# Performance work log

Hardware: AMD Instinct MI355X
Metric: run time of the kernel (lower is better)

## Reference

```python
import jax, jax.numpy as jnp
import numpy as np
from jax import lax

N, C_IN, H, W = 32, 128, 64, 64
C_OUT, KH, KW = 256, 3, 3
C_DIM = 64


def setup_inputs() -> dict:
    key = jax.random.key(0)
    k1, k2, k3, k4, k5 = jax.random.split(key, 5)
    return {
        "x": jax.random.normal(k1, (N, C_IN, H, W), dtype=jnp.float32),
        "c": jax.random.normal(k2, (N, C_DIM), dtype=jnp.float32),
        "weight": jax.random.normal(k3, (C_OUT, C_IN, KH, KW), dtype=jnp.float32),
        "c_weight": jax.random.normal(k4, (C_OUT, C_DIM), dtype=jnp.float32),
        "bias": jax.random.normal(k5, (C_OUT,), dtype=jnp.float32),
    }


def reference(x, c, weight, c_weight, bias):
    # Equivalent to the module's unfold + matmul path (groups=1, dilation=1,
    # zero padding=1, stride=1): a direct conv fused with the spatially
    # invariant context bias c @ c_weight^T and the channel bias.
    out = lax.conv_general_dilated(
        x, weight,
        window_strides=(1, 1),
        padding=((1, 1), (1, 1)),
        dimension_numbers=("NCHW", "OIHW", "NCHW"),
    )  # (N, C_out, H, W)
    ctx = jnp.einsum("nd,od->no", c, c_weight)  # (N, C_out), same at every spatial loc
    return out + ctx[:, :, None, None] + bias[None, :, None, None]
```

## Files before the change

### kernel.cpp

```cpp
#include <hip/hip_runtime.h>
#include <hip/hip_bf16.h>


#define NN   32
#define CIN  128
#define HH   64
#define WW   64
#define COUT 256
#define CDIM 64
#define HP   66
#define WP   66

#define XP_BYTES  ((size_t)NN*HP*WP*CIN*2)
#define WT_BYTES  ((size_t)9*COUT*CIN*2)
#define CTX_BYTES ((size_t)NN*COUT*4)
#define WS_NEEDED (XP_BYTES + WT_BYTES + CTX_BYTES)

typedef __attribute__((ext_vector_type(8))) short short8;
typedef __attribute__((ext_vector_type(4))) float float4v;

__device__ __forceinline__ void async16(const void* g, void* l) {
    __builtin_amdgcn_global_load_lds(
        (const __attribute__((address_space(1))) unsigned int*)g,
        (__attribute__((address_space(3))) unsigned int*)l, 16, 0, 0);
}

__global__ __launch_bounds__(256) void prep_x(const float* __restrict__ x,
                                              __hip_bfloat16* __restrict__ xP) {
    __shared__ float tile[CIN][WW + 1];
    int n = blockIdx.x >> 6;
    int h = blockIdx.x & 63;
    int t = threadIdx.x;
    const float* xp = x + ((size_t)n * CIN) * (HH * WW) + h * WW;
    int w = t & 63, cib = t >> 6;
    #pragma unroll
    for (int i = 0; i < 32; ++i) {
        int ci = cib + i * 4;
        tile[ci][w] = xp[(size_t)ci * (HH * WW) + w];
    }
    __syncthreads();
    int w2 = t >> 2, cseg = (t & 3) * 32;
    __hip_bfloat16* dst = xP + (((size_t)n * HP + (h + 1)) * WP + (w2 + 1)) * CIN + cseg;
    #pragma unroll
    for (int j = 0; j < 32; ++j)
        dst[j] = __float2bfloat16(tile[cseg + j][w2]);
}

__global__ __launch_bounds__(256) void prep_w(const float* __restrict__ wgt,
                                              __hip_bfloat16* __restrict__ wT) {
    int idx = blockIdx.x * 256 + threadIdx.x;
    int ci  = idx & 127;
    int co  = (idx >> 7) & 255;
    int tap = idx >> 15;
    wT[idx] = __float2bfloat16(wgt[((size_t)co * CIN + ci) * 9 + tap]);
}

__global__ __launch_bounds__(256) void prep_ctx(const float* __restrict__ c,
                                                const float* __restrict__ cw,
                                                const float* __restrict__ bias,
                                                float* __restrict__ ctx) {
    int idx = blockIdx.x * 256 + threadIdx.x;
    int co = idx & 255, n = idx >> 8;
    float a = bias[co];
    #pragma unroll 8
    for (int d = 0; d < CDIM; ++d) a += c[n * CDIM + d] * cw[co * CDIM + d];
    ctx[idx] = a;
}

__global__ __launch_bounds__(256) void conv_mfma(
    const __hip_bfloat16* __restrict__ xP,
    const __hip_bfloat16* __restrict__ wT,
    const float* __restrict__ ctx,
    float* __restrict__ out)
{
    __shared__ __align__(16) short A_s[4096];
    __shared__ __align__(16) short B_s[4096];

    int bid = blockIdx.x;
    int nt  = bid & 1;
    int mt  = bid >> 1;
    int n   = mt >> 5;
    int h0  = (mt & 31) << 1;

    int tid = threadIdx.x;
    int lane = tid & 63, wv = tid >> 6;
    int m0 = (wv & 1) * 64, n0 = (wv >> 1) * 64;

    int prow = wv * 32 + (lane >> 2);
    int cseg = (lane & 3) * 8;

    float4v acc[4][4] = {};

    for (int kh = 0; kh < 3; ++kh)
    for (int kw = 0; kw < 3; ++kw) {
        int tap = kh * 3 + kw;
        for (int kb = 0; kb < 4; ++kb) {
            __syncthreads();
            #pragma unroll
            for (int i = 0; i < 2; ++i) {
                int p  = prow + i * 16;
                int hh = h0 + (p >> 6) + kh;
                int ww = (p & 63) + kw;
                const __hip_bfloat16* asrc =
                    xP + (((size_t)n * HP + hh) * WP + ww) * CIN + kb * 32 + cseg;
                async16(asrc, &A_s[p * 32 + cseg]);
                const __hip_bfloat16* bsrc =
                    wT + ((size_t)tap * COUT + nt * 128 + p) * CIN + kb * 32 + cseg;
                async16(bsrc, &B_s[p * 32 + cseg]);
            }
            __syncthreads();

            short8 aF[4], bF[4];
            #pragma unroll
            for (int mi = 0; mi < 4; ++mi)
                aF[mi] = *(const short8*)&A_s[(m0 + mi * 16 + (lane & 15)) * 32 + (lane >> 4) * 8];
            #pragma unroll
            for (int ni = 0; ni < 4; ++ni)
                bF[ni] = *(const short8*)&B_s[(n0 + ni * 16 + (lane & 15)) * 32 + (lane >> 4) * 8];
            #pragma unroll
            for (int mi = 0; mi < 4; ++mi)
                #pragma unroll
                for (int ni = 0; ni < 4; ++ni)
                    acc[mi][ni] = __builtin_amdgcn_mfma_f32_16x16x32_bf16(
                        aF[mi], bF[ni], acc[mi][ni], 0, 0, 0);
        }
    }

    #pragma unroll
    for (int ni = 0; ni < 4; ++ni) {
        int co = nt * 128 + n0 + ni * 16 + (lane & 15);
        float cv = ctx[n * COUT + co];
        #pragma unroll
        for (int mi = 0; mi < 4; ++mi) {
            int rp = m0 + mi * 16 + (lane >> 4) * 4;
            int hh = h0 + (rp >> 6);
            int ww = rp & 63;
            float4v v = acc[mi][ni] + cv;
            *(float4v*)&out[(((size_t)n * COUT + co) * HH + hh) * WW + ww] = v;
        }
    }
}

__global__ __launch_bounds__(256) void contextual_conv_f32(
    const float* __restrict__ x, const float* __restrict__ c,
    const float* __restrict__ wgt, const float* __restrict__ cw,
    const float* __restrict__ bias, float* __restrict__ out)
{
    int idx = blockIdx.x * 256 + threadIdx.x;
    int w = idx & 63, h = (idx >> 6) & 63, cb = (idx >> 12) & 63, n = idx >> 18;
    float acc[4];
    #pragma unroll
    for (int j = 0; j < 4; ++j) acc[j] = bias[cb + j * 64];
    const float* cp = c + n * CDIM;
    for (int d = 0; d < CDIM; ++d) {
        float cv = cp[d];
        #pragma unroll
        for (int j = 0; j < 4; ++j) acc[j] += cv * cw[(cb + j * 64) * CDIM + d];
    }
    const float* xn = x + (size_t)n * (CIN * HH * WW);
    for (int ci = 0; ci < CIN; ++ci) {
        const float* xc = xn + ci * (HH * WW);
        float wv[4][9];
        #pragma unroll
        for (int j = 0; j < 4; ++j) {
            const float* wp = wgt + ((cb + j * 64) * CIN + ci) * 9;
            #pragma unroll
            for (int k = 0; k < 9; ++k) wv[j][k] = wp[k];
        }
        #pragma unroll
        for (int kh = 0; kh < 3; ++kh) {
            int hh = h + kh - 1;
            if (hh < 0 || hh >= HH) continue;
            const float* xr = xc + hh * WW;
            #pragma unroll
            for (int kw = 0; kw < 3; ++kw) {
                int ww = w + kw - 1;
                if (ww < 0 || ww >= WW) continue;
                float xv = xr[ww];
                #pragma unroll
                for (int j = 0; j < 4; ++j) acc[j] += xv * wv[j][kh * 3 + kw];
            }
        }
    }
    size_t obase = (size_t)n * (COUT * HH * WW) + (size_t)h * WW + w;
    #pragma unroll
    for (int j = 0; j < 4; ++j)
        out[obase + (size_t)(cb + j * 64) * (HH * WW)] = acc[j];
}

extern "C" void kernel_launch(void* const* d_in, const int* in_sizes, int n_in,
                              void* d_out, int out_size, void* d_ws, size_t ws_size,
                              hipStream_t stream) {
    const float* x    = (const float*)d_in[0];
    const float* c    = (const float*)d_in[1];
    const float* wgt  = (const float*)d_in[2];
    const float* cw   = (const float*)d_in[3];
    const float* bias = (const float*)d_in[4];
    float* out = (float*)d_out;

    if (ws_size < WS_NEEDED) {
        const int total_threads = NN * 64 * HH * WW;
        contextual_conv_f32<<<total_threads / 256, 256, 0, stream>>>(x, c, wgt, cw, bias, out);
        return;
    }

    char* ws = (char*)d_ws;
    __hip_bfloat16* xP = (__hip_bfloat16*)ws;
    __hip_bfloat16* wT = (__hip_bfloat16*)(ws + XP_BYTES);
    float*          cx = (float*)(ws + XP_BYTES + WT_BYTES);

    hipMemsetAsync(ws, 0, XP_BYTES, stream);
    prep_x  <<<NN * HH, 256, 0, stream>>>(x, xP);
    prep_w  <<<(9 * COUT * CIN) / 256, 256, 0, stream>>>(wgt, wT);
    prep_ctx<<<(NN * COUT) / 256, 256, 0, stream>>>(c, cw, bias, cx);
    conv_mfma<<<2048, 256, 0, stream>>>(xP, wT, cx, out);
}
```

Baseline: 293.8 us.

## Swizzle LDS tiles to avoid bank conflicts and vectorize input transpose

The conv kernel now stores A and B tiles in LDS with an XOR swizzle on the 16-byte chunk index. The global source offset is permuted so the LDS destination stays linear, as global_load_lds requires, and fragment reads use a matching swizzled column to cut bank conflicts on the short8 loads. The prep_x transpose now reads x with float4 vector loads and writes eight bf16 values per 16-byte store instead of scalar stores. The swizzle must stay consistent between the fill and read sides, or the MFMA operands will be wrong.

```diff
diff --git a/kernel.cpp b/kernel.cpp
--- a/kernel.cpp
+++ b/kernel.cpp
@@ -27,23 +27,36 @@
 
 __global__ __launch_bounds__(256) void prep_x(const float* __restrict__ x,
                                               __hip_bfloat16* __restrict__ xP) {
-    __shared__ float tile[CIN][WW + 1];
+    __shared__ float tile[CIN][65];
     int n = blockIdx.x >> 6;
     int h = blockIdx.x & 63;
     int t = threadIdx.x;
-    const float* xp = x + ((size_t)n * CIN) * (HH * WW) + h * WW;
-    int w = t & 63, cib = t >> 6;
-    #pragma unroll
-    for (int i = 0; i < 32; ++i) {
-        int ci = cib + i * 4;
-        tile[ci][w] = xp[(size_t)ci * (HH * WW) + w];
+    const float* xb = x + (size_t)n * CIN * HH * WW + (size_t)h * WW;
+
+    int lane16 = t & 15, rgrp = t >> 4;
+    #pragma unroll
+    for (int i = 0; i < 8; ++i) {
+        int ci = rgrp + i * 16;
+        float4v v = *(const float4v*)(xb + (size_t)ci * (HH * WW) + lane16 * 4);
+        int w0 = lane16 * 4;
+        tile[ci][w0]     = v.x;
+        tile[ci][w0 + 1] = v.y;
+        tile[ci][w0 + 2] = v.z;
+        tile[ci][w0 + 3] = v.w;
     }
     __syncthreads();
-    int w2 = t >> 2, cseg = (t & 3) * 32;
-    __hip_bfloat16* dst = xP + (((size_t)n * HP + (h + 1)) * WP + (w2 + 1)) * CIN + cseg;
-    #pragma unroll
-    for (int j = 0; j < 32; ++j)
-        dst[j] = __float2bfloat16(tile[cseg + j][w2]);
+
+    int oct = t & 3, w = t >> 2;
+    __hip_bfloat16* db = xP + (((size_t)n * HP + (h + 1)) * WP + (w + 1)) * CIN;
+    #pragma unroll
+    for (int p = 0; p < 4; ++p) {
+        int ci0 = p * 32 + oct * 8;
+        union { short8 v; __hip_bfloat16 b[8]; } u;
+        #pragma unroll
+        for (int j = 0; j < 8; ++j)
+            u.b[j] = __float2bfloat16(tile[ci0 + j][w]);
+        *(short8*)(db + ci0) = u.v;
+    }
 }
 
 __global__ __launch_bounds__(256) void prep_w(const float* __restrict__ wgt,
@@ -87,7 +100,9 @@
     int m0 = (wv & 1) * 64, n0 = (wv >> 1) * 64;
 
     int prow = wv * 32 + (lane >> 2);
-    int cseg = (lane & 3) * 8;
+    int pdst = (lane & 3) * 8;
+    int qsrc = ((lane & 3) ^ ((lane >> 3) & 3)) * 8;
+    int pc = (((lane >> 4) ^ (((lane & 15) >> 1) & 3))) * 8;
 
     float4v acc[4][4] = {};
 
@@ -102,21 +117,21 @@
                 int hh = h0 + (p >> 6) + kh;
                 int ww = (p & 63) + kw;
                 const __hip_bfloat16* asrc =
-                    xP + (((size_t)n * HP + hh) * WP + ww) * CIN + kb * 32 + cseg;
-                async16(asrc, &A_s[p * 32 + cseg]);
+                    xP + (((size_t)n * HP + hh) * WP + ww) * CIN + kb * 32 + qsrc;
+                async16(asrc, &A_s[p * 32 + pdst]);
                 const __hip_bfloat16* bsrc =
-                    wT + ((size_t)tap * COUT + nt * 128 + p) * CIN + kb * 32 + cseg;
-                async16(bsrc, &B_s[p * 32 + cseg]);
+                    wT + ((size_t)tap * COUT + nt * 128 + p) * CIN + kb * 32 + qsrc;
+                async16(bsrc, &B_s[p * 32 + pdst]);
             }
             __syncthreads();
 
             short8 aF[4], bF[4];
             #pragma unroll
             for (int mi = 0; mi < 4; ++mi)
-                aF[mi] = *(const short8*)&A_s[(m0 + mi * 16 + (lane & 15)) * 32 + (lane >> 4) * 8];
+                aF[mi] = *(const short8*)&A_s[(m0 + mi * 16 + (lane & 15)) * 32 + pc];
             #pragma unroll
             for (int ni = 0; ni < 4; ++ni)
-                bF[ni] = *(const short8*)&B_s[(n0 + ni * 16 + (lane & 15)) * 32 + (lane >> 4) * 8];
+                bF[ni] = *(const short8*)&B_s[(n0 + ni * 16 + (lane & 15)) * 32 + pc];
             #pragma unroll
             for (int mi = 0; mi < 4; ++mi)
                 #pragma unroll
```

New measurement: 285.7 us. 2.8% less time.
